# Performance work log

Hardware: AMD Instinct MI355X
Metric: run time of the kernel (lower is better)

Reference implementation:

```python
import jax, jax.numpy as jnp
import numpy as np

N0, N1, N2, N3 = 524288, 262144, 65536, 8192
E0, E1, E2 = 2621440, 655360, 81920
D_IN, D_H, D_OUT = 256, 256, 64


def setup_inputs() -> dict:
    key = jax.random.key(0)
    ks = jax.random.split(key, 16)
    s = 0.02
    inp = {
        "x": jax.random.normal(ks[0], (N0, D_IN), dtype=jnp.float32),
        "src0": jax.random.randint(ks[1], (E0,), 0, N0, dtype=jnp.int32),
        "dst0": jax.random.randint(ks[2], (E0,), 0, N1, dtype=jnp.int32),
        "src1": jax.random.randint(ks[3], (E1,), 0, N1, dtype=jnp.int32),
        "dst1": jax.random.randint(ks[4], (E1,), 0, N2, dtype=jnp.int32),
        "src2": jax.random.randint(ks[5], (E2,), 0, N2, dtype=jnp.int32),
        "dst2": jax.random.randint(ks[6], (E2,), 0, N3, dtype=jnp.int32),
        "nd0": N1, "nd1": N2, "nd2": N3,
        "Wfc": jax.random.normal(ks[7], (D_IN, D_H), dtype=jnp.float32) * s,
        "bfc": jnp.zeros((D_H,), dtype=jnp.float32),
        "Ws0": jax.random.normal(ks[8], (D_H, D_H), dtype=jnp.float32) * s,
        "Wn0": jax.random.normal(ks[9], (D_H, D_H), dtype=jnp.float32) * s,
        "b0": jnp.zeros((D_H,), dtype=jnp.float32),
        "Ws1": jax.random.normal(ks[10], (D_H, D_H), dtype=jnp.float32) * s,
        "Wn1": jax.random.normal(ks[11], (D_H, D_H), dtype=jnp.float32) * s,
        "b1": jnp.zeros((D_H,), dtype=jnp.float32),
        "Ws2": jax.random.normal(ks[12], (D_H, D_OUT), dtype=jnp.float32) * s,
        "Wn2": jax.random.normal(ks[13], (D_H, D_OUT), dtype=jnp.float32) * s,
        "b2": jnp.zeros((D_OUT,), dtype=jnp.float32),
    }
    return inp


def sage_conv(h, src, dst, n_dst, Ws, Wn, b):
    # DGL SAGEConv 'mean': out = h_dst @ W_self + mean_neigh(h_src) @ W_neigh + b
    h_dst = h[:n_dst]
    msg = jnp.take(h, src, axis=0)                    # [E, d] gather
    agg = jax.ops.segment_sum(msg, dst, num_segments=n_dst)
    cnt = jax.ops.segment_sum(jnp.ones((dst.shape[0],), h.dtype), dst, num_segments=n_dst)
    mean = agg / jnp.maximum(cnt, 1.0)[:, None]
    return h_dst @ Ws + mean @ Wn + b


def reference(x, src0, dst0, src1, dst1, src2, dst2, nd0, nd1, nd2,
              Wfc, bfc, Ws0, Wn0, b0, Ws1, Wn1, b1, Ws2, Wn2, b2):
    h = jax.nn.relu(x @ Wfc + bfc)                    # input projection (dropout=0 -> identity)
    h = jax.nn.relu(sage_conv(h, src0, dst0, nd0, Ws0, Wn0, b0))
    h = jax.nn.relu(sage_conv(h, src1, dst1, nd1, Ws1, Wn1, b1))
    h = sage_conv(h, src2, dst2, nd2, Ws2, Wn2, b2)   # no activation on final layer
    return h
```

## Files before the change

### kernel.cpp

```cpp
#include <hip/hip_runtime.h>

constexpr int N0c = 524288, N1c = 262144, N2c = 65536, N3c = 8192;
constexpr int NTOT = N1c + N2c + N3c;

typedef __attribute__((ext_vector_type(8))) short   bf16x8;
typedef __attribute__((ext_vector_type(4))) float   f32x4;
typedef __attribute__((ext_vector_type(8))) unsigned short u16x8;

__device__ inline unsigned short f2bf(float f) {
    union { float f; unsigned u; } v; v.f = f;
    unsigned r = v.u + 0x7FFF + ((v.u >> 16) & 1);
    return (unsigned short)(r >> 16);
}
__device__ inline float bf2f(unsigned short u) {
    union { unsigned u; float f; } v; v.u = ((unsigned)u) << 16;
    return v.f;
}

__device__ inline void glds16(const void* g, void* l) {
    __builtin_amdgcn_global_load_lds(
        (const __attribute__((address_space(1))) unsigned int*)g,
        (__attribute__((address_space(3))) unsigned int*)l, 16, 0, 0);
}

struct WPack { const float* w[7]; unsigned short* o[7]; };

__global__ __launch_bounds__(256)
void wconv_all(WPack p, int* __restrict__ hist)
{
    if (blockIdx.x >= 1408) {
        const int zid = (blockIdx.x - 1408) * 256 + threadIdx.x;
        ((int4*)hist)[zid] = make_int4(0, 0, 0, 0);
        return;
    }
    const int idx = blockIdx.x * 256 + threadIdx.x;
    int widx, off, N;
    if (idx < 327680) { widx = idx >> 16; off = idx & 65535; N = 256; }
    else {
        const int r = idx - 327680;
        widx = 5 + (r >> 14); off = r & 16383; N = 64;
        if (widx > 6) return;
    }
    const int k = off / N, n = off % N;
    p.o[widx][n * 256 + k] = f2bf(p.w[widx][off]);
}

__device__ inline bf16x8 pack_bf8(const float* p) {
    const f32x4 u = *(const f32x4*)p;
    const f32x4 v = *(const f32x4*)(p + 4);
    bf16x8 t;
    #pragma unroll
    for (int j = 0; j < 4; ++j) {
        t[j]     = (short)f2bf(u[j]);
        t[j + 4] = (short)f2bf(v[j]);
    }
    return t;
}

template<int NT, int KC, bool DUAL, bool RELU, bool A_F32, bool OUT_BF16>
__global__ __launch_bounds__(512, 2)
void gemm2(const void* __restrict__ A1v, const void* __restrict__ A2v,
           const unsigned short* __restrict__ Wt1,
           const unsigned short* __restrict__ Wt2,
           const float* __restrict__ bias, void* __restrict__ Cv)
{
    constexpr int N     = NT * 16;
    constexpr int PH    = 256 / KC;
    constexpr int SLOTS = KC / 8;
    constexpr int GPM   = N * SLOTS;
    constexpr int TOTG  = GPM * (DUAL ? 2 : 1);
    static_assert(TOTG == 4096, "LDS sizing");
    __shared__ unsigned short Bs[TOTG * 8];

    const int t    = threadIdx.x;
    const int lane = t & 63;
    const int wv   = t >> 6;
    const int col  = lane & 15;
    const int kg   = lane >> 4;
    const int swz  = (col & 7) << 3;
    const long row0 = (long)blockIdx.x * 128 + wv * 16;

    const unsigned short* A1h = (const unsigned short*)A1v;
    const float*          A1f = (const float*)A1v;
    const unsigned short* A2h = (const unsigned short*)A2v;

    f32x4 acc[NT];
    #pragma unroll
    for (int nt = 0; nt < NT; ++nt) acc[nt] = (f32x4){0.f, 0.f, 0.f, 0.f};

    const long ar = (row0 + col) * 256;

    for (int kh = 0; kh < PH; ++kh) {
        if (kh) __syncthreads();
        #pragma unroll
        for (int it = 0; it < TOTG / 512; ++it) {
            const int g  = it * 512 + t;
            const int m  = DUAL ? (g / GPM) : 0;
            const int gm = DUAL ? (g % GPM) : g;
            const int n  = gm / SLOTS;
            const int s  = gm % SLOTS;
            const int ss = s ^ (n & 7);
            const unsigned short* srcb =
                (m ? Wt2 : Wt1) + n * 256 + kh * KC + ss * 8;
            glds16(srcb, &Bs[(it * 512 + wv * 64) * 8]);
        }
        __syncthreads();

        #pragma unroll
        for (int k0 = 0; k0 < KC; k0 += 32) {
            const int kx = (k0 + kg * 8) ^ swz;
            const long ac = ar + kh * KC + k0 + kg * 8;
            bf16x8 a1, a2;
            if constexpr (A_F32) a1 = pack_bf8(&A1f[ac]);
            else                 a1 = *(const bf16x8*)&A1h[ac];
            if constexpr (DUAL)  a2 = *(const bf16x8*)&A2h[ac];
            #pragma unroll
            for (int nt = 0; nt < NT; ++nt) {
                const bf16x8 b1 = *(const bf16x8*)&Bs[(nt * 16 + col) * KC + kx];
                acc[nt] = __builtin_amdgcn_mfma_f32_16x16x32_bf16(a1, b1, acc[nt], 0, 0, 0);
                if constexpr (DUAL) {
                    const bf16x8 b2 = *(const bf16x8*)&Bs[GPM * 8 + (nt * 16 + col) * KC + kx];
                    acc[nt] = __builtin_amdgcn_mfma_f32_16x16x32_bf16(a2, b2, acc[nt], 0, 0, 0);
                }
            }
        }
    }

    #pragma unroll
    for (int nt = 0; nt < NT; ++nt) {
        const int c = nt * 16 + col;
        const float bb = bias[c];
        #pragma unroll
        for (int rr = 0; rr < 4; ++rr) {
            const long row = row0 + kg * 4 + rr;
            float o = acc[nt][rr] + bb;
            if constexpr (RELU) o = fmaxf(o, 0.f);
            if constexpr (OUT_BF16)
                ((unsigned short*)Cv)[row * N + c] = f2bf(o);
            else
                ((float*)Cv)[row * N + c] = o;
        }
    }
}

struct CsrArgs {
    const int* src0; const int* dst0;
    const int* src1; const int* dst1;
    const int* src2; const int* dst2;
    int e0, e01, etot;
};

__global__ __launch_bounds__(256)
void rank_k(CsrArgs a, int* __restrict__ hist, int* __restrict__ rank)
{
    const int i = blockIdx.x * 256 + threadIdx.x;
    if (i >= a.etot) return;
    const int* dstp; int e, hb;
    if (i < a.e0)       { dstp = a.dst0; e = i;         hb = 0; }
    else if (i < a.e01) { dstp = a.dst1; e = i - a.e0;  hb = N1c; }
    else                { dstp = a.dst2; e = i - a.e01; hb = N1c + N2c; }
    rank[i] = atomicAdd(&hist[hb + dstp[e]], 1);
}

__global__ __launch_bounds__(256)
void scan1_k(const int* __restrict__ hist, int* __restrict__ offs,
             int* __restrict__ bsum, int n)
{
    __shared__ int sm[256];
    const int t = threadIdx.x;
    const int base = blockIdx.x * 1024 + t * 4;
    int4 v = make_int4(0, 0, 0, 0);
    if (base < n) v = *(const int4*)&hist[base];
    const int s = v.x + v.y + v.z + v.w;
    int val = s;
    sm[t] = val; __syncthreads();
    #pragma unroll
    for (int off = 1; off < 256; off <<= 1) {
        const int add = (t >= off) ? sm[t - off] : 0;
        __syncthreads();
        val += add;
        sm[t] = val;
        __syncthreads();
    }
    const int excl = val - s;
    if (base < n) {
        offs[base]     = excl;
        offs[base + 1] = excl + v.x;
        offs[base + 2] = excl + v.x + v.y;
        offs[base + 3] = excl + v.x + v.y + v.z;
    }
    if (t == 255) bsum[blockIdx.x] = val;
}

__global__ __launch_bounds__(512)
void scan2_k(int* __restrict__ bsum, int nb)
{
    __shared__ int sm[512];
    const int t = threadIdx.x;
    const int s = (t < nb) ? bsum[t] : 0;
    int val = s;
    sm[t] = val; __syncthreads();
    #pragma unroll
    for (int off = 1; off < 512; off <<= 1) {
        const int add = (t >= off) ? sm[t - off] : 0;
        __syncthreads();
        val += add;
        sm[t] = val;
        __syncthreads();
    }
    if (t < nb) bsum[t] = val - s;
}

__global__ __launch_bounds__(256)
void scan3_k(int* __restrict__ offs, const int* __restrict__ bsum, int etot)
{
    const int i = blockIdx.x * 256 + threadIdx.x;
    offs[i] += bsum[i >> 10];
    if (i == 0) offs[NTOT] = etot;
}

__global__ __launch_bounds__(256)
void place_k(CsrArgs a, const int* __restrict__ offs, const int* __restrict__ rank,
             int* __restrict__ ssrc)
{
    const int i = blockIdx.x * 256 + threadIdx.x;
    if (i >= a.etot) return;
    const int* dstp; const int* srcp; int e, hb;
    if (i < a.e0)       { dstp = a.dst0; srcp = a.src0; e = i;         hb = 0; }
    else if (i < a.e01) { dstp = a.dst1; srcp = a.src1; e = i - a.e0;  hb = N1c; }
    else                { dstp = a.dst2; srcp = a.src2; e = i - a.e01; hb = N1c + N2c; }
    const int g = hb + dstp[e];
    ssrc[offs[g] + rank[i]] = srcp[e];
}

__global__ __launch_bounds__(256)
void agg_k(const unsigned short* __restrict__ h, const int* __restrict__ ssrc,
           const int* __restrict__ ob, unsigned short* __restrict__ agg, int n)
{
    const int w    = blockIdx.x * 4 + (threadIdx.x >> 6);
    const int lane = threadIdx.x & 63;
    if (w >= n) return;
    const int beg = ob[w];
    const int end = ob[w + 1];
    const int hf  = lane >> 5;
    const int co  = (lane & 31) * 8;

    float acc[8] = {0.f, 0.f, 0.f, 0.f, 0.f, 0.f, 0.f, 0.f};

    int j = beg;
    for (; j + 16 <= end; j += 16) {
        u16x8 v[8];
        #pragma unroll
        for (int q = 0; q < 8; ++q)
            v[q] = *(const u16x8*)&h[(size_t)ssrc[j + 2 * q + hf] * 256 + co];
        #pragma unroll
        for (int q = 0; q < 8; ++q)
            #pragma unroll
            for (int c = 0; c < 8; ++c) acc[c] += bf2f(v[q][c]);
    }
    const int rem = end - j;
    if (rem > 8) {
        u16x8 v[8]; bool ok[8];
        #pragma unroll
        for (int q = 0; q < 8; ++q) {
            const int e = j + 2 * q + hf;
            ok[q] = (e < end);
            v[q] = *(const u16x8*)&h[(size_t)ssrc[ok[q] ? e : (end - 1)] * 256 + co];
        }
        #pragma unroll
        for (int q = 0; q < 8; ++q)
            #pragma unroll
            for (int c = 0; c < 8; ++c) acc[c] += ok[q] ? bf2f(v[q][c]) : 0.0f;
    } else if (rem > 0) {
        u16x8 v[4]; bool ok[4];
        #pragma unroll
        for (int q = 0; q < 4; ++q) {
            const int e = j + 2 * q + hf;
            ok[q] = (e < end);
            v[q] = *(const u16x8*)&h[(size_t)ssrc[ok[q] ? e : (end - 1)] * 256 + co];
        }
        #pragma unroll
        for (int q = 0; q < 4; ++q)
            #pragma unroll
            for (int c = 0; c < 8; ++c) acc[c] += ok[q] ? bf2f(v[q][c]) : 0.0f;
    }

    #pragma unroll
    for (int c = 0; c < 8; ++c) acc[c] += __shfl_xor(acc[c], 32);

    if (hf == 0) {
        const float inv = 1.0f / fmaxf((float)(end - beg), 1.0f);
        u16x8 o;
        #pragma unroll
        for (int c = 0; c < 8; ++c) o[c] = f2bf(acc[c] * inv);
        *(u16x8*)&agg[(size_t)w * 256 + co] = o;
    }
}

extern "C" void kernel_launch(void* const* d_in, const int* in_sizes, int n_in,
                              void* d_out, int out_size, void* d_ws, size_t ws_size,
                              hipStream_t stream)
{
    const float* x    = (const float*)d_in[0];
    const int*   src0 = (const int*)d_in[1];
    const int*   dst0 = (const int*)d_in[2];
    const int*   src1 = (const int*)d_in[3];
    const int*   dst1 = (const int*)d_in[4];
    const int*   src2 = (const int*)d_in[5];
    const int*   dst2 = (const int*)d_in[6];
    const float* Wfc  = (const float*)d_in[10];
    const float* bfc  = (const float*)d_in[11];
    const float* Ws0  = (const float*)d_in[12];
    const float* Wn0  = (const float*)d_in[13];
    const float* b0   = (const float*)d_in[14];
    const float* Ws1  = (const float*)d_in[15];
    const float* Wn1  = (const float*)d_in[16];
    const float* b1   = (const float*)d_in[17];
    const float* Ws2  = (const float*)d_in[18];
    const float* Wn2  = (const float*)d_in[19];
    const float* b2   = (const float*)d_in[20];
    const int E0 = in_sizes[1], E1 = in_sizes[3], E2 = in_sizes[5];
    const int Etot = E0 + E1 + E2;

    char* ws = (char*)d_ws;
    unsigned short* h0   = (unsigned short*)ws;
    unsigned short* h1   = (unsigned short*)(ws + (256ULL << 20));
    unsigned short* h2   = (unsigned short*)(ws + (384ULL << 20));
    unsigned short* agg  = (unsigned short*)(ws + (416ULL << 20));
    unsigned short* Wt   = (unsigned short*)(ws + (544ULL << 20));
    int*            hist = (int*)(ws + (545ULL << 20));
    int*            offs = (int*)(ws + (547ULL << 20));
    int*            bsum = (int*)(ws + (549ULL << 20));
    int*            ssrc = (int*)(ws + (550ULL << 20));
    int*            rank = (int*)(ws + (564ULL << 20));

    unsigned short* wfc = Wt;
    unsigned short* ws0 = Wt + 65536;
    unsigned short* wn0 = Wt + 131072;
    unsigned short* ws1 = Wt + 196608;
    unsigned short* wn1 = Wt + 262144;
    unsigned short* ws2 = Wt + 327680;
    unsigned short* wn2 = Wt + 344064;

    const dim3 blk(256);

    WPack wp;
    wp.w[0] = Wfc; wp.w[1] = Ws0; wp.w[2] = Wn0; wp.w[3] = Ws1; wp.w[4] = Wn1;
    wp.w[5] = Ws2; wp.w[6] = Wn2;
    wp.o[0] = wfc; wp.o[1] = ws0; wp.o[2] = wn0; wp.o[3] = ws1; wp.o[4] = wn1;
    wp.o[5] = ws2; wp.o[6] = wn2;
    wconv_all<<<dim3(1408 + 328), blk, 0, stream>>>(wp, hist);

    CsrArgs ca;
    ca.src0 = src0; ca.dst0 = dst0; ca.src1 = src1; ca.dst1 = dst1;
    ca.src2 = src2; ca.dst2 = dst2;
    ca.e0 = E0; ca.e01 = E0 + E1; ca.etot = Etot;
    rank_k<<<dim3((Etot + 255) / 256), blk, 0, stream>>>(ca, hist, rank);
    scan1_k<<<dim3(NTOT / 1024), blk, 0, stream>>>(hist, offs, bsum, NTOT);
    scan2_k<<<dim3(1), dim3(512), 0, stream>>>(bsum, NTOT / 1024);
    scan3_k<<<dim3(NTOT / 256), blk, 0, stream>>>(offs, bsum, Etot);
    place_k<<<dim3((Etot + 255) / 256), blk, 0, stream>>>(ca, offs, rank, ssrc);

    gemm2<16, 128, false, true, true, true><<<dim3(N0c / 128), dim3(512), 0, stream>>>(
        x, nullptr, wfc, nullptr, bfc, h0);

    agg_k<<<dim3(N1c / 4), blk, 0, stream>>>(h0, ssrc, offs, agg, N1c);
    gemm2<16, 64, true, true, false, true><<<dim3(N1c / 128), dim3(512), 0, stream>>>(
        h0, agg, ws0, wn0, b0, h1);

    agg_k<<<dim3(N2c / 4), blk, 0, stream>>>(h1, ssrc, offs + N1c, agg, N2c);
    gemm2<16, 64, true, true, false, true><<<dim3(N2c / 128), dim3(512), 0, stream>>>(
        h1, agg, ws1, wn1, b1, h2);

    agg_k<<<dim3(N3c / 4), blk, 0, stream>>>(h2, ssrc, offs + N1c + N2c, agg, N3c);
    gemm2<4, 256, true, false, false, false><<<dim3(N3c / 128), dim3(512), 0, stream>>>(
        h2, agg, ws2, wn2, b2, (float*)d_out);
}
```

Before: 850.7 us.

## Fuse input-projection GEMM with edge rank/histogram atomics in one launch

Merges the first dense projection GEMM and the edge histogram/rank kernel into a single launch, with block index deciding which role each block plays. The memory-bound atomic histogram work can then overlap with the compute-heavy GEMM, and one launch is removed. The GEMM launch is moved ahead of the scan kernels, which do not depend on its output. The rank blocks now allocate the GEMM's LDS and use its launch bounds, which may reduce how many of them are resident at once.

```diff
diff --git a/kernel.cpp b/kernel.cpp
--- a/kernel.cpp
+++ b/kernel.cpp
@@ -55,6 +55,83 @@
         t[j + 4] = (short)f2bf(v[j]);
     }
     return t;
+}
+
+struct CsrArgs {
+    const int* src0; const int* dst0;
+    const int* src1; const int* dst1;
+    const int* src2; const int* dst2;
+    int e0, e01, etot;
+};
+
+__global__ __launch_bounds__(512, 2)
+void fc_rank_k(const float* __restrict__ A1f, const unsigned short* __restrict__ Wt1,
+               const float* __restrict__ bias, unsigned short* __restrict__ Cv,
+               CsrArgs a, int* __restrict__ hist, int* __restrict__ rank,
+               int gemmBlocks)
+{
+    if ((int)blockIdx.x >= gemmBlocks) {
+        const int i = ((int)blockIdx.x - gemmBlocks) * 512 + (int)threadIdx.x;
+        if (i >= a.etot) return;
+        const int* dstp; int e, hb;
+        if (i < a.e0)       { dstp = a.dst0; e = i;         hb = 0; }
+        else if (i < a.e01) { dstp = a.dst1; e = i - a.e0;  hb = N1c; }
+        else                { dstp = a.dst2; e = i - a.e01; hb = N1c + N2c; }
+        rank[i] = atomicAdd(&hist[hb + dstp[e]], 1);
+        return;
+    }
+
+    constexpr int KC = 128, SLOTS = KC / 8, GPM = 256 * SLOTS;
+    __shared__ unsigned short Bs[GPM * 8];
+
+    const int t    = threadIdx.x;
+    const int lane = t & 63;
+    const int wv   = t >> 6;
+    const int col  = lane & 15;
+    const int kg   = lane >> 4;
+    const int swz  = (col & 7) << 3;
+    const long row0 = (long)blockIdx.x * 128 + wv * 16;
+
+    f32x4 acc[16];
+    #pragma unroll
+    for (int nt = 0; nt < 16; ++nt) acc[nt] = (f32x4){0.f, 0.f, 0.f, 0.f};
+
+    const long ar = (row0 + col) * 256;
+
+    for (int kh = 0; kh < 2; ++kh) {
+        if (kh) __syncthreads();
+        #pragma unroll
+        for (int it = 0; it < GPM / 512; ++it) {
+            const int g  = it * 512 + t;
+            const int n  = g / SLOTS;
+            const int s  = g % SLOTS;
+            const int ss = s ^ (n & 7);
+            glds16(Wt1 + n * 256 + kh * KC + ss * 8, &Bs[(it * 512 + wv * 64) * 8]);
+        }
+        __syncthreads();
+
+        #pragma unroll
+        for (int k0 = 0; k0 < KC; k0 += 32) {
+            const int kx = (k0 + kg * 8) ^ swz;
+            const bf16x8 a1 = pack_bf8(&A1f[ar + kh * KC + k0 + kg * 8]);
+            #pragma unroll
+            for (int nt = 0; nt < 16; ++nt) {
+                const bf16x8 b1 = *(const bf16x8*)&Bs[(nt * 16 + col) * KC + kx];
+                acc[nt] = __builtin_amdgcn_mfma_f32_16x16x32_bf16(a1, b1, acc[nt], 0, 0, 0);
+            }
+        }
+    }
+
+    #pragma unroll
+    for (int nt = 0; nt < 16; ++nt) {
+        const int c = nt * 16 + col;
+        const float bb = bias[c];
+        #pragma unroll
+        for (int rr = 0; rr < 4; ++rr) {
+            const long row = row0 + kg * 4 + rr;
+            Cv[row * 256 + c] = f2bf(fmaxf(acc[nt][rr] + bb, 0.f));
+        }
+    }
 }
 
 template<int NT, int KC, bool DUAL, bool RELU, bool A_F32, bool OUT_BF16>
@@ -141,25 +218,6 @@
                 ((float*)Cv)[row * N + c] = o;
         }
     }
-}
-
-struct CsrArgs {
-    const int* src0; const int* dst0;
-    const int* src1; const int* dst1;
-    const int* src2; const int* dst2;
-    int e0, e01, etot;
-};
-
-__global__ __launch_bounds__(256)
-void rank_k(CsrArgs a, int* __restrict__ hist, int* __restrict__ rank)
-{
-    const int i = blockIdx.x * 256 + threadIdx.x;
-    if (i >= a.etot) return;
-    const int* dstp; int e, hb;
-    if (i < a.e0)       { dstp = a.dst0; e = i;         hb = 0; }
-    else if (i < a.e01) { dstp = a.dst1; e = i - a.e0;  hb = N1c; }
-    else                { dstp = a.dst2; e = i - a.e01; hb = N1c + N2c; }
-    rank[i] = atomicAdd(&hist[hb + dstp[e]], 1);
 }
 
 __global__ __launch_bounds__(256)
@@ -355,15 +413,16 @@
     ca.src0 = src0; ca.dst0 = dst0; ca.src1 = src1; ca.dst1 = dst1;
     ca.src2 = src2; ca.dst2 = dst2;
     ca.e0 = E0; ca.e01 = E0 + E1; ca.etot = Etot;
-    rank_k<<<dim3((Etot + 255) / 256), blk, 0, stream>>>(ca, hist, rank);
+    const int gemmBlocks = N0c / 128;
+    const int rankBlocks = (Etot + 511) / 512;
+    fc_rank_k<<<dim3(gemmBlocks + rankBlocks), dim3(512), 0, stream>>>(
+        x, wfc, bfc, h0, ca, hist, rank, gemmBlocks);
+
     scan1_k<<<dim3(NTOT / 1024), blk, 0, stream>>>(hist, offs, bsum, NTOT);
     scan2_k<<<dim3(1), dim3(512), 0, stream>>>(bsum, NTOT / 1024);
     scan3_k<<<dim3(NTOT / 256), blk, 0, stream>>>(offs, bsum, Etot);
     place_k<<<dim3((Etot + 255) / 256), blk, 0, stream>>>(ca, offs, rank, ssrc);
 
-    gemm2<16, 128, false, true, true, true><<<dim3(N0c / 128), dim3(512), 0, stream>>>(
-        x, nullptr, wfc, nullptr, bfc, h0);
-
     agg_k<<<dim3(N1c / 4), blk, 0, stream>>>(h0, ssrc, offs, agg, N1c);
     gemm2<16, 64, true, true, false, true><<<dim3(N1c / 128), dim3(512), 0, stream>>>(
         h0, agg, ws0, wn0, b0, h1);
```

New measurement: 846.2 us (median of 2 runs). About the same (-0.5%).
